# Kernel optimization log

Hardware: AMD Instinct MI355X
Metric: run time of the kernel (lower is better)

The kernel has to match this reference:

```python
import jax, jax.numpy as jnp
import numpy as np
from jax import lax

B, CIN, HF, WF = 8, 512, 60, 60      # encoder feature
NCLS = 19                            # seg out channels
PATCH = 10                           # patch_size
DEPTH = 8                            # 2**att_depth
UPS = 8                              # seg upsampling
HI = HF * UPS                        # 480 upsampled image size
NP_IMG = (HI // PATCH) ** 2          # 2304 image patches
NP_FEA = (HI // DEPTH // PATCH) ** 2 # 36 feature patches
POOL_SIZES = (1, 2, 3, 6)


def resize_ac(x, H, W):
    # bilinear, align_corners=True (matches F.interpolate/UpsamplingBilinear2d)
    b, c, h, w = x.shape
    ys = jnp.arange(H, dtype=x.dtype) * ((h - 1) / max(H - 1, 1))
    xs = jnp.arange(W, dtype=x.dtype) * ((w - 1) / max(W - 1, 1))
    y0 = jnp.floor(ys).astype(jnp.int32); y1 = jnp.minimum(y0 + 1, h - 1)
    x0 = jnp.floor(xs).astype(jnp.int32); x1 = jnp.minimum(x0 + 1, w - 1)
    wy = (ys - y0.astype(x.dtype))[:, None]
    wx = (xs - x0.astype(x.dtype))[None, :]
    g = lambda yi, xi: x[:, :, yi[:, None], xi[None, :]]
    top = (1 - wx) * g(y0, x0) + wx * g(y0, x1)
    bot = (1 - wx) * g(y1, x0) + wx * g(y1, x1)
    return (1 - wy) * top + wy * bot


def bn_eval(x, gamma, beta, mean, var, eps=1e-5):
    s = lambda v: v[None, :, None, None]
    return (x - s(mean)) * (s(gamma) / jnp.sqrt(s(var) + eps)) + s(beta)


def setup_inputs() -> dict:
    key = jax.random.key(0)
    ks = jax.random.split(key, 16)
    f32 = jnp.float32
    return {
        "feat": jax.random.normal(ks[0], (B, CIN, HF, WF), f32),
        "attentions": jax.random.normal(ks[1], (B, NCLS, NP_IMG, NP_FEA), f32),
        "w_psp": jax.random.normal(ks[2], (4, CIN // 4, CIN), f32) * 0.03,
        "b_psp0": jax.random.normal(ks[3], (CIN // 4,), f32) * 0.02,
        "bn_psp_gamma": jax.random.uniform(ks[4], (3, CIN // 4), f32, 0.5, 1.5),
        "bn_psp_beta": jax.random.normal(ks[5], (3, CIN // 4), f32) * 0.02,
        "bn_psp_mean": jax.random.normal(ks[6], (3, CIN // 4), f32) * 0.02,
        "bn_psp_var": jax.random.uniform(ks[7], (3, CIN // 4), f32, 0.5, 1.5),
        "w_conv": jax.random.normal(ks[8], (512, 2 * CIN), f32) * 0.03,
        "bn_conv_gamma": jax.random.uniform(ks[9], (512,), f32, 0.5, 1.5),
        "bn_conv_beta": jax.random.normal(ks[10], (512,), f32) * 0.02,
        "bn_conv_mean": jax.random.normal(ks[11], (512,), f32) * 0.02,
        "bn_conv_var": jax.random.uniform(ks[12], (512,), f32, 0.5, 1.5),
        "w_segconv": jax.random.normal(ks[13], (NCLS, 512, 3, 3), f32) * 0.03,
        "b_segconv": jax.random.normal(ks[14], (NCLS,), f32) * 0.02,
    }


def _forward(feat, attentions, w_psp, b_psp0, bn_psp_gamma, bn_psp_beta,
             bn_psp_mean, bn_psp_var, w_conv, bn_conv_gamma, bn_conv_beta,
             bn_conv_mean, bn_conv_var, w_segconv, b_segconv):
    # ---- PSP pyramid ----
    branches = []
    for i, p in enumerate(POOL_SIZES):
        k = HF // p
        pooled = feat.reshape(B, CIN, p, k, p, k).mean(axis=(3, 5))  # adaptive avg pool
        y = jnp.einsum('oc,bchw->bohw', w_psp[i], pooled)
        if i == 0:  # pool_size==1 -> no BN, conv has bias
            y = y + b_psp0[None, :, None, None]
        else:
            y = bn_eval(y, bn_psp_gamma[i-1], bn_psp_beta[i-1],
                        bn_psp_mean[i-1], bn_psp_var[i-1])
        y = jax.nn.relu(y)
        branches.append(resize_ac(y, HF, WF))
    x = jnp.concatenate(branches + [feat], axis=1)  # [B, 2*CIN, HF, WF]

    # ---- 1x1 Conv2dReLU + BN (eval), dropout is identity in eval ----
    x = jnp.einsum('oc,bchw->bohw', w_conv, x)
    x = jax.nn.relu(bn_eval(x, bn_conv_gamma, bn_conv_beta, bn_conv_mean, bn_conv_var))

    # ---- SegmentationHead ----
    x = lax.conv_general_dilated(x, w_segconv, (1, 1), 'SAME',
                                 dimension_numbers=('NCHW', 'OIHW', 'NCHW'))
    x = x + b_segconv[None, :, None, None]
    x = resize_ac(x, HI, HI)  # [B, NCLS, 480, 480]

    # one-hot of per-pixel argmax (scatter of ones)
    am = jnp.argmax(x, axis=1)
    x_softmax = (am[:, None] == jnp.arange(NCLS)[None, :, None, None]).astype(x.dtype)

    # grouped ones-conv stride 8 / 64 == 8x8 average pooling
    hf = HI // DEPTH  # 60
    argx_feamap = x_softmax.reshape(B, NCLS, hf, DEPTH, hf, DEPTH).mean(axis=(3, 5))

    # unfold(k=10, s=10): [B, C, 36, 100] (blocks row-major, patch row-major)
    nb = hf // PATCH  # 6
    unf = argx_feamap.reshape(B, NCLS, nb, PATCH, nb, PATCH)
    unf = unf.transpose(0, 1, 2, 4, 3, 5).reshape(B, NCLS, nb * nb, PATCH * PATCH)

    counts = jnp.count_nonzero(attentions, axis=-1, keepdims=True).astype(x.dtype) + 1e-5
    att = jnp.einsum('bcpk,bckq->bcpq', attentions / counts, unf)  # [B,C,2304,100]

    # fold back to [B, C, 480, 480]
    nbi = HI // PATCH  # 48
    corr = att.reshape(B, NCLS, nbi, nbi, PATCH, PATCH)
    corr = corr.transpose(0, 1, 2, 4, 3, 5).reshape(B, NCLS, HI, HI)

    x = corr * x + x  # activation=None -> identity
    return x, attentions


def reference(feat, attentions, w_psp, b_psp0, bn_psp_gamma, bn_psp_beta,
              bn_psp_mean, bn_psp_var, w_conv, bn_conv_gamma, bn_conv_beta,
              bn_conv_mean, bn_conv_var, w_segconv, b_segconv):
    return _forward(feat, attentions, w_psp, b_psp0, bn_psp_gamma, bn_psp_beta,
                    bn_psp_mean, bn_psp_var, w_conv, bn_conv_gamma, bn_conv_beta,
                    bn_conv_mean, bn_conv_var, w_segconv, b_segconv)
```

## Files before the change

kernel.cpp:

```cpp
#include <hip/hip_runtime.h>
#include <stdint.h>

#define NB 8
#define NCLS 19

typedef short s8v __attribute__((ext_vector_type(8)));
typedef float f4v __attribute__((ext_vector_type(4)));

__device__ __forceinline__ unsigned short f2b(float f){
  union { float f; uint32_t u; } v; v.f = f;
  uint32_t u = v.u;
  uint32_t r = (u + 0x7fffu + ((u >> 16) & 1u)) >> 16;
  return (unsigned short)r;
}

#define GLOAD16(g, l) __builtin_amdgcn_global_load_lds( \
    (const __attribute__((address_space(1))) unsigned int*)(g), \
    (__attribute__((address_space(3))) unsigned int*)(l), 16, 0, 0)

#define OFF_X512 0
#define OFF_POOL 31490048
#define OFF_Z    32309248
#define OFF_BNS  33128448
#define OFF_BNB  33130496
#define OFF_SEG  33132544
#define OFF_ARGX 35321344
#define OFF_WSEG 37510144
#define OFF_WF   37805056

__global__ void k_halo(unsigned short* __restrict__ x512p){
  int idx = blockIdx.x*256 + threadIdx.x;
  if (idx >= 124928) return;
  int pix = idx >> 6;
  int ch  = (idx & 63) << 3;
  int b = pix / 244;
  int r = pix - b*244;
  int h, w;
  if (r < 62){ h = 0; w = r; }
  else if (r < 124){ h = 61; w = r - 62; }
  else if (r < 184){ h = r - 124 + 1; w = 0; }
  else { h = r - 184 + 1; w = 61; }
  s8v z = (s8v){0,0,0,0,0,0,0,0};
  *(s8v*)(x512p + (((size_t)b*62 + h)*62 + w)*512 + ch) = z;
}

__global__ void k0_copy(const float4* __restrict__ in, float4* __restrict__ out, int n4){
  for (int i = blockIdx.x*blockDim.x + threadIdx.x; i < n4; i += gridDim.x*blockDim.x)
    out[i] = in[i];
}

__global__ void kprep(const float* __restrict__ wseg, unsigned short* __restrict__ wsegT){
  int idx = blockIdx.x*256 + threadIdx.x;
  if (idx >= 9*32*512) return;
  int tap = idx / (32*512);
  int rem = idx - tap*(32*512);
  int o = rem >> 9, c = rem & 511;
  float v = (o < NCLS) ? wseg[((size_t)o*512 + c)*9 + tap] : 0.0f;
  wsegT[idx] = f2b(v);
}

__global__ void kprep2(const float* __restrict__ wconv, unsigned short* __restrict__ wfT){
  int idx = blockIdx.x*256 + threadIdx.x;
  if (idx >= 512*512) return;
  int o = idx >> 9, c = idx & 511;
  wfT[idx] = f2b(wconv[(size_t)o*1024 + 512 + c]);
}

__global__ __launch_bounds__(256) void ktr(const float* __restrict__ feat, unsigned short* __restrict__ featT){
  __shared__ unsigned short lt[64*528];
  int px0 = blockIdx.x*64, b = blockIdx.y;
  for (int i = threadIdx.x; i < 64*512; i += 256){
    int c = i >> 6, px = i & 63;
    float v = feat[((size_t)b*512 + c)*3600 + min(px0+px, 3599)];
    lt[px*528 + c] = f2b(v);
  }
  __syncthreads();
  for (int i = threadIdx.x; i < 4096; i += 256){
    int px = i >> 6, c8 = i & 63;
    s8v v = *(const s8v*)(lt + px*528 + c8*8);
    *(s8v*)(featT + ((size_t)b*3712 + px0 + px)*512 + c8*8) = v;
  }
}

__global__ void kbn(const float* __restrict__ g, const float* __restrict__ be,
                    const float* __restrict__ m, const float* __restrict__ v,
                    float* __restrict__ sc, float* __restrict__ sh){
  int i = blockIdx.x*256 + threadIdx.x;
  if (i < 512){
    float s = g[i] * rsqrtf(v[i] + 1e-5f);
    sc[i] = s; sh[i] = be[i] - m[i]*s;
  }
}

__global__ __launch_bounds__(64) void k1_pool(const float* __restrict__ feat, float* __restrict__ pooled){
  int bc = blockIdx.x;
  __shared__ float rs[64][12];
  int r = threadIdx.x;
  if (r < 60){
    const float* row = feat + (size_t)bc*3600 + r*60;
    float s6[6];
    #pragma unroll
    for (int j = 0; j < 6; j++){
      float s = 0.f;
      #pragma unroll
      for (int i = 0; i < 10; i++) s += row[j*10+i];
      s6[j] = s;
    }
    float s3_0 = s6[0]+s6[1], s3_1 = s6[2]+s6[3], s3_2 = s6[4]+s6[5];
    float s2_0 = s3_0 + s6[2], s2_1 = s6[3] + s3_2;
    rs[r][0]  = s2_0 + s2_1;
    rs[r][1]  = s2_0; rs[r][2]  = s2_1;
    rs[r][3]  = s3_0; rs[r][4]  = s3_1; rs[r][5] = s3_2;
    #pragma unroll
    for (int j = 0; j < 6; j++) rs[r][6+j] = s6[j];
  }
  __syncthreads();
  int t = threadIdx.x;
  if (t < 50){
    int P, by, bx, jcol;
    if (t == 0){ P=1; by=0; bx=0; jcol=0; }
    else if (t < 5){ P=2; int l=t-1; by=l>>1; bx=l&1; jcol=1+bx; }
    else if (t < 14){ P=3; int l=t-5; by=l/3; bx=l-(l/3)*3; jcol=3+bx; }
    else { P=6; int l=t-14; by=l/6; bx=l-(l/6)*6; jcol=6+bx; }
    int k = 60/P;
    float s = 0.f;
    for (int rr = 0; rr < k; rr++) s += rs[by*k+rr][jcol];
    pooled[(size_t)bc*50 + t] = s * (1.0f/((float)k*(float)k));
  }
}

__global__ __launch_bounds__(256) void k2_branch(
    const float* __restrict__ pooled, const float* __restrict__ w_psp,
    const float* __restrict__ b_psp0,
    const float* __restrict__ png, const float* __restrict__ pnb,
    const float* __restrict__ pnm, const float* __restrict__ pnv,
    const float* __restrict__ wconv, float* __restrict__ zbuf)
{
  int bin = blockIdx.x % 50;
  int b   = blockIdx.x / 50;
  int br  = (bin < 1) ? 0 : (bin < 5) ? 1 : (bin < 14) ? 2 : 3;
  __shared__ float pl[512];
  __shared__ float ysh[128];
  int t = threadIdx.x;
  pl[t]       = pooled[((size_t)b*512 + t)*50 + bin];
  pl[t + 256] = pooled[((size_t)b*512 + t + 256)*50 + bin];
  __syncthreads();
  if (t < 128){
    const float* wr = w_psp + ((size_t)br*128 + t)*512;
    float s = 0.f;
    #pragma unroll 8
    for (int c = 0; c < 512; c++) s += pl[c]*wr[c];
    if (br == 0) s += b_psp0[t];
    else {
      int ib = (br-1)*128 + t;
      s = (s - pnm[ib]) * png[ib] * rsqrtf(pnv[ib] + 1e-5f) + pnb[ib];
    }
    ysh[t] = fmaxf(s, 0.f);
  }
  __syncthreads();
  for (int o = t; o < 512; o += 256){
    const float* wc = wconv + (size_t)o*1024 + br*128;
    float s = 0.f;
    #pragma unroll
    for (int c = 0; c < 128; c++) s += ysh[c]*wc[c];
    zbuf[((size_t)b*50 + bin)*512 + o] = s;
  }
}

__global__ __launch_bounds__(256) void k3_gemm(
    const unsigned short* __restrict__ featT, const unsigned short* __restrict__ wfT,
    const float* __restrict__ zbuf, const float* __restrict__ bns,
    const float* __restrict__ bnb, unsigned short* __restrict__ x512p)
{
  __shared__ unsigned short lmem[2*128*64];
  unsigned short* lA = lmem;
  unsigned short* lB = lmem + 128*64;

  const int t = threadIdx.x;
  const int lane = t & 63;
  const int wave = t >> 6;
  const int wm = wave >> 1;
  const int wn = wave & 1;
  const int pix0 = blockIdx.x * 128;
  const int o0   = blockIdx.y * 128;
  const int b    = blockIdx.z;

  f4v acc[4][4];
  #pragma unroll
  for (int i = 0; i < 4; i++)
    #pragma unroll
    for (int j = 0; j < 4; j++)
      acc[i][j] = (f4v){0.f,0.f,0.f,0.f};

  const int sub  = lane >> 3;
  const int slot = lane & 7;

  for (int kk = 0; kk < 8; kk++){
    #pragma unroll
    for (int j = 0; j < 4; j++){
      int px = j*32 + wave*8 + sub;
      int pix = min(pix0 + px, 3599);
      const unsigned short* src = featT + ((size_t)b*3712 + pix)*512 + kk*64 + ((slot ^ (px & 7)) << 3);
      GLOAD16(src, lA + j*2048 + wave*512);
    }
    #pragma unroll
    for (int j = 0; j < 4; j++){
      int o = j*32 + wave*8 + sub;
      const unsigned short* src = wfT + (size_t)(o0 + o)*512 + kk*64 + ((slot ^ (o & 7)) << 3);
      GLOAD16(src, lB + j*2048 + wave*512);
    }
    __syncthreads();
    #pragma unroll
    for (int ks = 0; ks < 2; ks++){
      const int chunk = ks*4 + (lane >> 4);
      s8v af[4], bg[4];
      #pragma unroll
      for (int mf = 0; mf < 4; mf++){
        int p = wm*64 + mf*16 + (lane & 15);
        af[mf] = *(s8v*)((char*)lA + p*128 + ((chunk ^ (p & 7)))*16);
      }
      #pragma unroll
      for (int nf = 0; nf < 4; nf++){
        int o = wn*64 + nf*16 + (lane & 15);
        bg[nf] = *(s8v*)((char*)lB + o*128 + ((chunk ^ (o & 7)))*16);
      }
      #pragma unroll
      for (int mf = 0; mf < 4; mf++)
        #pragma unroll
        for (int nf = 0; nf < 4; nf++)
          acc[mf][nf] = __builtin_amdgcn_mfma_f32_16x16x32_bf16(af[mf], bg[nf], acc[mf][nf], 0, 0, 0);
    }
    __syncthreads();
  }

  float* zl  = (float*)lmem;
  float* lsc = zl + 50*128;
  float* lsh = lsc + 128;
  for (int i = t; i < 50*128; i += 256){
    int bin = i >> 7, ol = i & 127;
    zl[i] = zbuf[((size_t)b*50 + bin)*512 + o0 + ol];
  }
  if (t < 128){ lsc[t] = bns[o0 + t]; lsh[t] = bnb[o0 + t]; }
  __syncthreads();

  #pragma unroll
  for (int mf = 0; mf < 4; mf++){
    #pragma unroll
    for (int r = 0; r < 4; r++){
      int p = pix0 + wm*64 + mf*16 + (lane >> 4)*4 + r;
      if (p >= 3600) continue;
      int h = p / 60, w = p - (p/60)*60;
      float wgt[3][4]; int bix[3][4];
      const int pbase[3] = {1,5,14};
      const int psz[3]   = {2,3,6};
      #pragma unroll
      for (int ib = 0; ib < 3; ib++){
        int P = psz[ib];
        float fy = (float)h * (float)(P-1) / 59.0f;
        float fx = (float)w * (float)(P-1) / 59.0f;
        int y0 = (int)fy; int y1 = min(y0+1, P-1); float wy = fy - (float)y0;
        int x0 = (int)fx; int x1 = min(x0+1, P-1); float wx = fx - (float)x0;
        bix[ib][0] = pbase[ib] + y0*P + x0; wgt[ib][0] = (1.f-wy)*(1.f-wx);
        bix[ib][1] = pbase[ib] + y0*P + x1; wgt[ib][1] = (1.f-wy)*wx;
        bix[ib][2] = pbase[ib] + y1*P + x0; wgt[ib][2] = wy*(1.f-wx);
        bix[ib][3] = pbase[ib] + y1*P + x1; wgt[ib][3] = wy*wx;
      }
      size_t obase = (((size_t)b*62 + (h+1))*62 + (w+1))*512 + o0;
      #pragma unroll
      for (int nf = 0; nf < 4; nf++){
        int ol = wn*64 + nf*16 + (lane & 15);
        float zs = zl[ol];
        #pragma unroll
        for (int ib = 0; ib < 3; ib++)
          #pragma unroll
          for (int tp = 0; tp < 4; tp++)
            zs += wgt[ib][tp] * zl[bix[ib][tp]*128 + ol];
        float v = acc[mf][nf][r] + zs;
        v = fmaxf(v * lsc[ol] + lsh[ol], 0.f);
        x512p[obase + ol] = f2b(v);
      }
    }
  }
}

__global__ __launch_bounds__(256) void k4_conv(
    const unsigned short* __restrict__ x512p, const unsigned short* __restrict__ wsegT,
    const float* __restrict__ bseg, float* __restrict__ seg60)
{
  __shared__ unsigned short lW[32*512];
  const int h = blockIdx.x;
  const int b = blockIdx.y;
  const int t = threadIdx.x;
  const int lane = t & 63;
  const int wave = t >> 6;
  const int wpix = wave*16 + (lane & 15);
  const int wld = min(wpix, 59);

  f4v acc[2];
  acc[0] = (f4v){0.f,0.f,0.f,0.f};
  acc[1] = (f4v){0.f,0.f,0.f,0.f};

  for (int tap = 0; tap < 9; tap++){
    __syncthreads();
    for (int i = t; i < 2048; i += 256){
      int orow = i >> 6;
      int cn = i & 63;
      s8v v = *(const s8v*)(wsegT + ((size_t)tap*32 + orow)*512 + cn*8);
      *(s8v*)((char*)lW + orow*1024 + ((cn ^ (orow & 7)))*16) = v;
    }
    __syncthreads();
    int dy = tap/3 - 1, dx = tap - (tap/3)*3 - 1;
    const unsigned short* arow = x512p + (((size_t)b*62 + (h+dy+1))*62 + (wld+dx+1))*512 + (lane>>4)*8;
    #pragma unroll 4
    for (int cs = 0; cs < 16; cs++){
      int cb = cs*32;
      s8v a = *(const s8v*)(arow + cb);
      #pragma unroll
      for (int nf = 0; nf < 2; nf++){
        int o = nf*16 + (lane & 15);
        int chunk = (cb >> 3) + (lane >> 4);
        s8v bv = *(s8v*)((char*)lW + o*1024 + ((chunk ^ (o & 7)))*16);
        acc[nf] = __builtin_amdgcn_mfma_f32_16x16x32_bf16(a, bv, acc[nf], 0, 0, 0);
      }
    }
  }
  #pragma unroll
  for (int nf = 0; nf < 2; nf++){
    int o = nf*16 + (lane & 15);
    if (o < NCLS){
      float bias = bseg[o];
      #pragma unroll
      for (int r = 0; r < 4; r++){
        int wst = wave*16 + (lane >> 4)*4 + r;
        if (wst < 60)
          seg60[(((size_t)b*60 + h)*60 + wst)*NCLS + o] = acc[nf][r] + bias;
      }
    }
  }
}

__global__ __launch_bounds__(256) void k5_argmax(const float* __restrict__ seg60, float* __restrict__ argx){
  int gw = blockIdx.x*4 + (threadIdx.x >> 6);
  int b = gw / 3600;
  int cell = gw - b*3600;
  int fy = cell / 60, fx = cell - (cell/60)*60;
  int lane = threadIdx.x & 63;
  int py = fy*8 + (lane >> 3), px = fx*8 + (lane & 7);
  float yy = (float)py * (59.0f/479.0f); int y0 = (int)yy; int y1 = min(y0+1, 59); float wy = yy - (float)y0;
  float xx = (float)px * (59.0f/479.0f); int x0 = (int)xx; int x1 = min(x0+1, 59); float wx = xx - (float)x0;
  const float* base = seg60 + (size_t)b*3600*NCLS;
  const float* s00 = base + (y0*60 + x0)*NCLS;
  const float* s01 = base + (y0*60 + x1)*NCLS;
  const float* s10 = base + (y1*60 + x0)*NCLS;
  const float* s11 = base + (y1*60 + x1)*NCLS;
  float w00 = (1.f-wy)*(1.f-wx), w01 = (1.f-wy)*wx, w10 = wy*(1.f-wx), w11 = wy*wx;
  float best = -3.0e38f; int bc = 0;
  #pragma unroll
  for (int c = 0; c < NCLS; c++){
    float v = w00*s00[c] + w01*s01[c] + w10*s10[c] + w11*s11[c];
    if (v > best){ best = v; bc = c; }
  }
  int cnt = 0;
  #pragma unroll
  for (int c = 0; c < NCLS; c++){
    unsigned long long m = __ballot(bc == c);
    if (lane == c) cnt = __popcll(m);
  }
  int ky = fy/10, qy = fy - (fy/10)*10, kx = fx/10, qx = fx - (fx/10)*10;
  int qidx = (ky*6+kx)*100 + qy*10 + qx;
  if (lane < NCLS)
    argx[((size_t)b*NCLS + lane)*3600 + qidx] = (float)cnt * (1.0f/64.0f);
}

__global__ __launch_bounds__(256) void k7_final(
    const float* __restrict__ att, const float* __restrict__ argx,
    const float* __restrict__ seg60, float* __restrict__ out)
{
  int pr = blockIdx.x, c = blockIdx.y, b = blockIdx.z;
  __shared__ float lds[7104];
  float* latA  = lds;
  float* U     = lds + 1920;
  float* corrl = lds;
  float* hrow  = lds + 4800;
  float* inv   = lds + 6784;
  float* srow  = lds + 6832;
  const int t = threadIdx.x;

  const float* ab = att + (((size_t)b*NCLS + c)*2304 + (size_t)pr*48)*36;
  for (int i = t; i < 432; i += 256){
    int pc = i/9, j = i - pc*9;
    *(f4v*)(latA + pc*40 + j*4) = *(const f4v*)(ab + pc*36 + j*4);
  }
  const f4v* ub4 = (const f4v*)(argx + ((size_t)b*NCLS + c)*3600);
  for (int i = t; i < 900; i += 256)
    ((f4v*)U)[i] = ub4[i];
  __syncthreads();

  int ybase;
  { float yy0 = (float)(pr*10) * (59.0f/479.0f); ybase = (int)yy0; }

  f4v acc[6];
  int tp = 0, tq = 0;
  if (t < 200){
    tp = t/25; tq = t - tp*25;
    #pragma unroll
    for (int r = 0; r < 6; r++) acc[r] = (f4v){0.f,0.f,0.f,0.f};
    #pragma unroll 4
    for (int k = 0; k < 36; k++){
      f4v u = *(const f4v*)(U + k*100 + tq*4);
      #pragma unroll
      for (int r = 0; r < 6; r++)
        acc[r] += latA[(tp*6+r)*40 + k] * u;
    }
  } else {
    int idx = t - 200;
    if (idx < 48){
      int nz = 0;
      #pragma unroll
      for (int k = 0; k < 36; k++) nz += (latA[idx*40+k] != 0.f) ? 1 : 0;
      inv[idx] = 1.0f / ((float)nz + 1e-5f);
    }
    for (int i = idx; i < 240; i += 56){
      int j = i/60, x = i - (i/60)*60;
      int row = min(ybase + j, 59);
      srow[j*64 + x] = seg60[(((size_t)b*60 + row)*60 + x)*NCLS + c];
    }
  }
  __syncthreads();

  if (t < 200){
    #pragma unroll
    for (int r = 0; r < 6; r++){
      int pc = tp*6 + r;
      *(f4v*)(corrl + pc*100 + tq*4) = acc[r] * inv[pc];
    }
  }
  for (int i = t; i < 1920; i += 256){
    int j = i/480, px = i - j*480;
    float xx = (float)px * (59.0f/479.0f);
    int x0 = (int)xx; int x1 = min(x0+1, 59); float wx = xx - (float)x0;
    hrow[j*480 + px] = (1.f-wx)*srow[j*64 + x0] + wx*srow[j*64 + x1];
  }
  __syncthreads();

  float* outb = out + ((size_t)b*NCLS + c)*230400 + (size_t)pr*4800;
  for (int qy = 0; qy < 10; qy++){
    int py = pr*10 + qy;
    float yy = (float)py * (59.0f/479.0f);
    int y0 = (int)yy; int y1 = min(y0+1, 59); float wy = yy - (float)y0;
    const float* h0 = hrow + (y0 - ybase)*480;
    const float* h1 = hrow + (y1 - ybase)*480;
    float omw = 1.f - wy;
    for (int px = t; px < 480; px += 256){
      float xv = omw*h0[px] + wy*h1[px];
      int pc = (px*6554) >> 16;
      int qx = px - pc*10;
      float corr = corrl[pc*100 + qy*10 + qx];
      outb[qy*480 + px] = xv * (1.f + corr);
    }
  }
}

extern "C" void kernel_launch(void* const* d_in, const int* in_sizes, int n_in,
                              void* d_out, int out_size, void* d_ws, size_t ws_size,
                              hipStream_t stream)
{
  (void)in_sizes; (void)n_in; (void)out_size; (void)ws_size;
  const float* feat   = (const float*)d_in[0];
  const float* attn   = (const float*)d_in[1];
  const float* w_psp  = (const float*)d_in[2];
  const float* b_psp0 = (const float*)d_in[3];
  const float* png    = (const float*)d_in[4];
  const float* pnb    = (const float*)d_in[5];
  const float* pnm    = (const float*)d_in[6];
  const float* pnv    = (const float*)d_in[7];
  const float* wconv  = (const float*)d_in[8];
  const float* cg     = (const float*)d_in[9];
  const float* cbt    = (const float*)d_in[10];
  const float* cm     = (const float*)d_in[11];
  const float* cv     = (const float*)d_in[12];
  const float* wseg   = (const float*)d_in[13];
  const float* bseg   = (const float*)d_in[14];

  float* out1 = (float*)d_out;
  float* out2 = out1 + (size_t)35020800;

  char* ws = (char*)d_ws;
  unsigned short* x512p = (unsigned short*)(ws + OFF_X512);
  float* pooled = (float*)(ws + OFF_POOL);
  float* zbuf   = (float*)(ws + OFF_Z);
  float* bns    = (float*)(ws + OFF_BNS);
  float* bnb    = (float*)(ws + OFF_BNB);
  float* seg60  = (float*)(ws + OFF_SEG);
  float* argx   = (float*)(ws + OFF_ARGX);
  unsigned short* wsegT = (unsigned short*)(ws + OFF_WSEG);
  unsigned short* wfT   = (unsigned short*)(ws + OFF_WF);
  unsigned short* featT = (unsigned short*)d_out;

  k_halo<<<488, 256, 0, stream>>>(x512p);
  kprep<<<576, 256, 0, stream>>>(wseg, wsegT);
  kprep2<<<1024, 256, 0, stream>>>(wconv, wfT);
  ktr<<<dim3(57,8), 256, 0, stream>>>(feat, featT);
  kbn<<<2, 256, 0, stream>>>(cg, cbt, cm, cv, bns, bnb);
  k1_pool<<<4096, 64, 0, stream>>>(feat, pooled);
  k2_branch<<<400, 256, 0, stream>>>(pooled, w_psp, b_psp0, png, pnb, pnm, pnv, wconv, zbuf);
  k3_gemm<<<dim3(29,4,8), 256, 0, stream>>>(featT, wfT, zbuf, bns, bnb, x512p);
  k0_copy<<<2048, 256, 0, stream>>>((const float4*)attn, (float4*)out2, 12607488/4);
  k4_conv<<<dim3(60,8), 256, 0, stream>>>(x512p, wsegT, bseg, seg60);
  k5_argmax<<<7200, 256, 0, stream>>>(seg60, argx);
  k7_final<<<dim3(48,19,8), 256, 0, stream>>>(attn, argx, seg60, out1);
}
```

Measured before the change: 300.8 us.

## Use bf16 MFMA for attention-correction GEMM and merge setup kernels

The per-block attention×unfolded-argmax product in the final kernel moves from scalar fp32 FMAs to bf16 16x16x32 MFMA. The argmax map is stored transposed, zero-padded and XOR-swizzled in bf16 so it can be loaded straight into LDS with global_load_lds. The five small setup kernels (halo zeroing, weight conversions, feature transpose, BN fold) are merged into one launch that also zeroes the padded argmax buffer. This cuts ALU work, LDS footprint and launch overhead, at the cost of bf16 rounding of the attention weights and the correction term.

```diff
diff --git a/kernel.cpp b/kernel.cpp
--- a/kernel.cpp
+++ b/kernel.cpp
@@ -28,68 +28,94 @@
 #define OFF_WSEG 37510144
 #define OFF_WF   37805056
 
-__global__ void k_halo(unsigned short* __restrict__ x512p){
-  int idx = blockIdx.x*256 + threadIdx.x;
-  if (idx >= 124928) return;
-  int pix = idx >> 6;
-  int ch  = (idx & 63) << 3;
-  int b = pix / 244;
-  int r = pix - b*244;
-  int h, w;
-  if (r < 62){ h = 0; w = r; }
-  else if (r < 124){ h = 61; w = r - 62; }
-  else if (r < 184){ h = r - 124 + 1; w = 0; }
-  else { h = r - 184 + 1; w = 61; }
-  s8v z = (s8v){0,0,0,0,0,0,0,0};
-  *(s8v*)(x512p + (((size_t)b*62 + h)*62 + w)*512 + ch) = z;
+__global__ __launch_bounds__(256) void k_setup(
+    const float* __restrict__ feat, unsigned short* __restrict__ featT,
+    unsigned short* __restrict__ x512p,
+    const float* __restrict__ wseg, unsigned short* __restrict__ wsegT,
+    const float* __restrict__ wconv, unsigned short* __restrict__ wfT,
+    const float* __restrict__ g, const float* __restrict__ be,
+    const float* __restrict__ m, const float* __restrict__ v,
+    float* __restrict__ sc, float* __restrict__ sh,
+    unsigned short* __restrict__ argxT)
+{
+  __shared__ unsigned short lt[64*528];
+  int bid = blockIdx.x;
+  if (bid < 456){
+    int b = bid / 57, px0 = (bid - b*57)*64;
+    for (int i = threadIdx.x; i < 64*512; i += 256){
+      int c = i >> 6, px = i & 63;
+      float val = feat[((size_t)b*512 + c)*3600 + min(px0+px, 3599)];
+      lt[px*528 + c] = f2b(val);
+    }
+    __syncthreads();
+    for (int i = threadIdx.x; i < 4096; i += 256){
+      int px = i >> 6, c8 = i & 63;
+      s8v vv = *(const s8v*)(lt + px*528 + c8*8);
+      *(s8v*)(featT + ((size_t)b*3712 + px0 + px)*512 + c8*8) = vv;
+    }
+    return;
+  }
+  bid -= 456;
+  if (bid < 488){
+    int idx = bid*256 + threadIdx.x;
+    if (idx < 124928){
+      int pix = idx >> 6;
+      int ch  = (idx & 63) << 3;
+      int b = pix / 244;
+      int r = pix - b*244;
+      int h, w;
+      if (r < 62){ h = 0; w = r; }
+      else if (r < 124){ h = 61; w = r - 62; }
+      else if (r < 184){ h = r - 124 + 1; w = 0; }
+      else { h = r - 184 + 1; w = 61; }
+      s8v z = (s8v){0,0,0,0,0,0,0,0};
+      *(s8v*)(x512p + (((size_t)b*62 + h)*62 + w)*512 + ch) = z;
+    }
+    return;
+  }
+  bid -= 488;
+  if (bid < 576){
+    int idx = bid*256 + threadIdx.x;
+    if (idx < 9*32*512){
+      int tap = idx / (32*512);
+      int rem = idx - tap*(32*512);
+      int o = rem >> 9, c = rem & 511;
+      float val = (o < NCLS) ? wseg[((size_t)o*512 + c)*9 + tap] : 0.0f;
+      wsegT[idx] = f2b(val);
+    }
+    return;
+  }
+  bid -= 576;
+  if (bid < 1024){
+    int idx = bid*256 + threadIdx.x;
+    if (idx < 512*512){
+      int o = idx >> 9, c = idx & 511;
+      wfT[idx] = f2b(wconv[(size_t)o*1024 + 512 + c]);
+    }
+    return;
+  }
+  bid -= 1024;
+  if (bid < 2){
+    int i = bid*256 + threadIdx.x;
+    if (i < 512){
+      float s = g[i] * rsqrtf(v[i] + 1e-5f);
+      sc[i] = s; sh[i] = be[i] - m[i]*s;
+    }
+    return;
+  }
+  bid -= 2;
+  {
+    int gi = bid*256 + threadIdx.x;
+    if (gi < 136192){
+      s8v z = (s8v){0,0,0,0,0,0,0,0};
+      ((s8v*)argxT)[gi] = z;
+    }
+  }
 }
 
 __global__ void k0_copy(const float4* __restrict__ in, float4* __restrict__ out, int n4){
   for (int i = blockIdx.x*blockDim.x + threadIdx.x; i < n4; i += gridDim.x*blockDim.x)
     out[i] = in[i];
-}
-
-__global__ void kprep(const float* __restrict__ wseg, unsigned short* __restrict__ wsegT){
-  int idx = blockIdx.x*256 + threadIdx.x;
-  if (idx >= 9*32*512) return;
-  int tap = idx / (32*512);
-  int rem = idx - tap*(32*512);
-  int o = rem >> 9, c = rem & 511;
-  float v = (o < NCLS) ? wseg[((size_t)o*512 + c)*9 + tap] : 0.0f;
-  wsegT[idx] = f2b(v);
-}
-
-__global__ void kprep2(const float* __restrict__ wconv, unsigned short* __restrict__ wfT){
-  int idx = blockIdx.x*256 + threadIdx.x;
-  if (idx >= 512*512) return;
-  int o = idx >> 9, c = idx & 511;
-  wfT[idx] = f2b(wconv[(size_t)o*1024 + 512 + c]);
-}
-
-__global__ __launch_bounds__(256) void ktr(const float* __restrict__ feat, unsigned short* __restrict__ featT){
-  __shared__ unsigned short lt[64*528];
-  int px0 = blockIdx.x*64, b = blockIdx.y;
-  for (int i = threadIdx.x; i < 64*512; i += 256){
-    int c = i >> 6, px = i & 63;
-    float v = feat[((size_t)b*512 + c)*3600 + min(px0+px, 3599)];
-    lt[px*528 + c] = f2b(v);
-  }
-  __syncthreads();
-  for (int i = threadIdx.x; i < 4096; i += 256){
-    int px = i >> 6, c8 = i & 63;
-    s8v v = *(const s8v*)(lt + px*528 + c8*8);
-    *(s8v*)(featT + ((size_t)b*3712 + px0 + px)*512 + c8*8) = v;
-  }
-}
-
-__global__ void kbn(const float* __restrict__ g, const float* __restrict__ be,
-                    const float* __restrict__ m, const float* __restrict__ v,
-                    float* __restrict__ sc, float* __restrict__ sh){
-  int i = blockIdx.x*256 + threadIdx.x;
-  if (i < 512){
-    float s = g[i] * rsqrtf(v[i] + 1e-5f);
-    sc[i] = s; sh[i] = be[i] - m[i]*s;
-  }
 }
 
 __global__ __launch_bounds__(64) void k1_pool(const float* __restrict__ feat, float* __restrict__ pooled){
@@ -339,7 +365,7 @@
   }
 }
 
-__global__ __launch_bounds__(256) void k5_argmax(const float* __restrict__ seg60, float* __restrict__ argx){
+__global__ __launch_bounds__(256) void k5_argmax(const float* __restrict__ seg60, unsigned short* __restrict__ argxT){
   int gw = blockIdx.x*4 + (threadIdx.x >> 6);
   int b = gw / 3600;
   int cell = gw - b*3600;
@@ -367,76 +393,103 @@
     if (lane == c) cnt = __popcll(m);
   }
   int ky = fy/10, qy = fy - (fy/10)*10, kx = fx/10, qx = fx - (fx/10)*10;
-  int qidx = (ky*6+kx)*100 + qy*10 + qx;
-  if (lane < NCLS)
-    argx[((size_t)b*NCLS + lane)*3600 + qidx] = (float)cnt * (1.0f/64.0f);
+  int q = qy*10 + qx, k = ky*6 + kx;
+  if (lane < NCLS){
+    unsigned short hv = f2b((float)cnt * (1.0f/64.0f));
+    argxT[(size_t)(b*NCLS + lane)*7168 + q*64 + (((k>>3) ^ (q&7))<<3) + (k&7)] = hv;
+  }
 }
 
 __global__ __launch_bounds__(256) void k7_final(
-    const float* __restrict__ att, const float* __restrict__ argx,
+    const float* __restrict__ att, const unsigned short* __restrict__ argxT,
     const float* __restrict__ seg60, float* __restrict__ out)
 {
   int pr = blockIdx.x, c = blockIdx.y, b = blockIdx.z;
-  __shared__ float lds[7104];
-  float* latA  = lds;
-  float* U     = lds + 1920;
-  float* corrl = lds;
-  float* hrow  = lds + 4800;
-  float* inv   = lds + 6784;
-  float* srow  = lds + 6832;
+  __shared__ char pool[30400];
+  unsigned short* Abf = (unsigned short*)pool;
+  unsigned short* Ubf = (unsigned short*)(pool + 6144);
+  float* corrl = (float*)pool;
+  float* hrow  = (float*)(pool + 21504);
+  float* inv   = (float*)(pool + 29184);
+  float* srow  = (float*)(pool + 29376);
   const int t = threadIdx.x;
+  const int lane = t & 63;
+  const int wave = t >> 6;
+
+  int ybase; { float yy0 = (float)(pr*10)*(59.0f/479.0f); ybase = (int)yy0; }
 
   const float* ab = att + (((size_t)b*NCLS + c)*2304 + (size_t)pr*48)*36;
-  for (int i = t; i < 432; i += 256){
-    int pc = i/9, j = i - pc*9;
-    *(f4v*)(latA + pc*40 + j*4) = *(const f4v*)(ab + pc*36 + j*4);
-  }
-  const f4v* ub4 = (const f4v*)(argx + ((size_t)b*NCLS + c)*3600);
-  for (int i = t; i < 900; i += 256)
-    ((f4v*)U)[i] = ub4[i];
-  __syncthreads();
-
-  int ybase;
-  { float yy0 = (float)(pr*10) * (59.0f/479.0f); ybase = (int)yy0; }
+  for (int i = t; i < 768; i += 256){
+    int pc = i >> 4, j = i & 15;
+    ushort4 w4 = make_ushort4(0,0,0,0);
+    if (j < 9){
+      f4v v = *(const f4v*)(ab + pc*36 + j*4);
+      w4.x = f2b(v[0]); w4.y = f2b(v[1]); w4.z = f2b(v[2]); w4.w = f2b(v[3]);
+    }
+    int ch = j >> 1;
+    *(ushort4*)((char*)Abf + pc*128 + (((ch ^ (pc & 7)))<<4) + (j & 1)*8) = w4;
+  }
+  {
+    const unsigned short* up = argxT + (size_t)(b*NCLS + c)*7168;
+    #pragma unroll
+    for (int r = 0; r < 4; r++){
+      int chunk0 = r*256 + wave*64;
+      if (chunk0 < 896)
+        GLOAD16(up + (size_t)(chunk0 + lane)*8, Ubf + (size_t)chunk0*8);
+    }
+  }
+  if (t < 240){
+    int j = t/60, x = t - (t/60)*60;
+    int row = min(ybase + j, 59);
+    srow[j*64 + x] = seg60[(((size_t)b*60 + row)*60 + x)*NCLS + c];
+  }
+  if (t < 48){
+    int nz = 0;
+    #pragma unroll
+    for (int j2 = 0; j2 < 9; j2++){
+      f4v v = *(const f4v*)(ab + t*36 + j2*4);
+      nz += (v[0]!=0.f)+(v[1]!=0.f)+(v[2]!=0.f)+(v[3]!=0.f);
+    }
+    inv[t] = 1.0f/((float)nz + 1e-5f);
+  }
+  __syncthreads();
 
   f4v acc[6];
-  int tp = 0, tq = 0;
-  if (t < 200){
-    tp = t/25; tq = t - tp*25;
-    #pragma unroll
-    for (int r = 0; r < 6; r++) acc[r] = (f4v){0.f,0.f,0.f,0.f};
-    #pragma unroll 4
-    for (int k = 0; k < 36; k++){
-      f4v u = *(const f4v*)(U + k*100 + tq*4);
-      #pragma unroll
-      for (int r = 0; r < 6; r++)
-        acc[r] += latA[(tp*6+r)*40 + k] * u;
-    }
-  } else {
-    int idx = t - 200;
-    if (idx < 48){
-      int nz = 0;
-      #pragma unroll
-      for (int k = 0; k < 36; k++) nz += (latA[idx*40+k] != 0.f) ? 1 : 0;
-      inv[idx] = 1.0f / ((float)nz + 1e-5f);
-    }
-    for (int i = idx; i < 240; i += 56){
-      int j = i/60, x = i - (i/60)*60;
-      int row = min(ybase + j, 59);
-      srow[j*64 + x] = seg60[(((size_t)b*60 + row)*60 + x)*NCLS + c];
-    }
-  }
-  __syncthreads();
-
-  if (t < 200){
-    #pragma unroll
-    for (int r = 0; r < 6; r++){
-      int pc = tp*6 + r;
-      *(f4v*)(corrl + pc*100 + tq*4) = acc[r] * inv[pc];
+  #pragma unroll
+  for (int s = 0; s < 6; s++) acc[s] = (f4v){0.f,0.f,0.f,0.f};
+  #pragma unroll
+  for (int s = 0; s < 6; s++){
+    int pi = wave + s*4;
+    if (pi < 21){
+      int M = pi/7, N = pi - (pi/7)*7;
+      #pragma unroll
+      for (int ks = 0; ks < 2; ks++){
+        int chunk = ks*4 + (lane >> 4);
+        int ar = M*16 + (lane & 15);
+        s8v af = *(s8v*)((char*)Abf + ar*128 + ((chunk ^ (ar & 7))<<4));
+        int qr = N*16 + (lane & 15);
+        s8v bg = *(s8v*)((char*)Ubf + qr*128 + ((chunk ^ (qr & 7))<<4));
+        acc[s] = __builtin_amdgcn_mfma_f32_16x16x32_bf16(af, bg, acc[s], 0, 0, 0);
+      }
+    }
+  }
+  __syncthreads();
+
+  #pragma unroll
+  for (int s = 0; s < 6; s++){
+    int pi = wave + s*4;
+    if (pi < 21){
+      int M = pi/7, N = pi - (pi/7)*7;
+      int q = N*16 + (lane & 15);
+      #pragma unroll
+      for (int r = 0; r < 4; r++){
+        int pc = M*16 + (lane >> 4)*4 + r;
+        corrl[pc*112 + q] = acc[s][r] * inv[pc];
+      }
     }
   }
   for (int i = t; i < 1920; i += 256){
-    int j = i/480, px = i - j*480;
+    int j = i/480, px = i - (i/480)*480;
     float xx = (float)px * (59.0f/479.0f);
     int x0 = (int)xx; int x1 = min(x0+1, 59); float wx = xx - (float)x0;
     hrow[j*480 + px] = (1.f-wx)*srow[j*64 + x0] + wx*srow[j*64 + x1];
@@ -455,7 +508,7 @@
       float xv = omw*h0[px] + wy*h1[px];
       int pc = (px*6554) >> 16;
       int qx = px - pc*10;
-      float corr = corrl[pc*100 + qy*10 + qx];
+      float corr = corrl[pc*112 + qy*10 + qx];
       outb[qy*480 + px] = xv * (1.f + corr);
     }
   }
@@ -492,21 +545,18 @@
   float* bns    = (float*)(ws + OFF_BNS);
   float* bnb    = (float*)(ws + OFF_BNB);
   float* seg60  = (float*)(ws + OFF_SEG);
-  float* argx   = (float*)(ws + OFF_ARGX);
+  unsigned short* argxT = (unsigned short*)(ws + OFF_ARGX);
   unsigned short* wsegT = (unsigned short*)(ws + OFF_WSEG);
   unsigned short* wfT   = (unsigned short*)(ws + OFF_WF);
   unsigned short* featT = (unsigned short*)d_out;
 
-  k_halo<<<488, 256, 0, stream>>>(x512p);
-  kprep<<<576, 256, 0, stream>>>(wseg, wsegT);
-  kprep2<<<1024, 256, 0, stream>>>(wconv, wfT);
-  ktr<<<dim3(57,8), 256, 0, stream>>>(feat, featT);
-  kbn<<<2, 256, 0, stream>>>(cg, cbt, cm, cv, bns, bnb);
+  k_setup<<<3078, 256, 0, stream>>>(feat, featT, x512p, wseg, wsegT, wconv, wfT,
+                                    cg, cbt, cm, cv, bns, bnb, argxT);
   k1_pool<<<4096, 64, 0, stream>>>(feat, pooled);
   k2_branch<<<400, 256, 0, stream>>>(pooled, w_psp, b_psp0, png, pnb, pnm, pnv, wconv, zbuf);
   k3_gemm<<<dim3(29,4,8), 256, 0, stream>>>(featT, wfT, zbuf, bns, bnb, x512p);
   k0_copy<<<2048, 256, 0, stream>>>((const float4*)attn, (float4*)out2, 12607488/4);
   k4_conv<<<dim3(60,8), 256, 0, stream>>>(x512p, wsegT, bseg, seg60);
-  k5_argmax<<<7200, 256, 0, stream>>>(seg60, argx);
-  k7_final<<<dim3(48,19,8), 256, 0, stream>>>(attn, argx, seg60, out1);
-}
+  k5_argmax<<<7200, 256, 0, stream>>>(seg60, argxT);
+  k7_final<<<dim3(48,19,8), 256, 0, stream>>>(attn, argxT, seg60, out1);
+}
```

Result: faster. 273.9 us (-8.9%).
